# Performance work log

Measured on AMD Instinct MI355X. Metric: run time of the kernel, lower is better.

## Reference

```python
import jax, jax.numpy as jnp
import numpy as np

# TT factorization: vocab = 8*8*8*8*16 = 65536, dim = 4^5 = 1024, rank 16
SHAPE = [(8, 4), (8, 4), (8, 4), (8, 4), (16, 4)]
RANKS = [1, 16, 16, 16, 16, 1]
VOCAB = 65536
DIM = 1024
BATCH, SEQ = 8, 2048


def setup_inputs() -> dict:
    key = jax.random.key(0)
    ks = jax.random.split(key, len(SHAPE) + 1)
    inp = {}
    for k, (n, m) in enumerate(SHAPE):
        core = jax.random.normal(ks[k], (RANKS[k], n * m, RANKS[k + 1]), dtype=jnp.float32) * 0.01
        inp[f"core{k}"] = core
    inp["indices"] = jax.random.randint(ks[-1], (BATCH, SEQ), 0, VOCAB)
    return inp


def _tt_full(cores):
    # Faithful port of tt_to_matrix: chain matmul of cores, then a flat reshape
    # to (VOCAB, DIM).  (The original code reshapes merged_shape -> (rows, cols)
    # directly, without the inverse interleave permute; we replicate that.)
    result = cores[0]  # (1, n0*m0, r1)
    for core in cores[1:]:
        r_prev = result.shape[-1]
        result = (result.reshape(-1, r_prev) @ core.reshape(r_prev, -1))
        result = result.reshape(1, -1, core.shape[-1])
    return result.reshape(VOCAB, DIM)


def reference(core0, core1, core2, core3, core4, indices):
    full = _tt_full([core0, core1, core2, core3, core4])  # (VOCAB, DIM)
    return jnp.take(full, indices, axis=0)              # (BATCH, SEQ, DIM)
```

## Files before the change

kernel.cpp:

```cpp
#include <hip/hip_runtime.h>
#include <hip/hip_fp16.h>


typedef float f32x4 __attribute__((ext_vector_type(4)));

#define RSTRIDE 20
#define GSTRIDE 328

__global__ __launch_bounds__(256) void tt_embed_kernel(
    const float* __restrict__ c0,
    const float* __restrict__ c1,
    const float* __restrict__ c2,
    const float* __restrict__ c3,
    const float* __restrict__ c4,
    const int*   __restrict__ idx,
    float*       __restrict__ out,
    int n_tokens)
{
    const int t   = threadIdx.x;
    const int tl  = t >> 5;
    const int l32 = t & 31;
    const int h   = (t >> 4) & 1;
    const int r   = t & 15;
    const int token = blockIdx.x * 8 + tl;
    const int v = (token < n_tokens) ? idx[token] : 0;

    __shared__ float w4s[8 * GSTRIDE];

    __half2 c4h[16][2];
    #pragma unroll
    for (int r4 = 0; r4 < 16; ++r4) {
        const float4 cv = *(const float4*)(c4 + (r4 << 6) + (r << 2));
        c4h[r4][0] = __floats2half2_rn(cv.x, cv.y);
        c4h[r4][1] = __floats2half2_rn(cv.z, cv.w);
    }

    float w2r = 0.f;
    {
        const int i0 = (v >> 11) & 31;
        const int i1 = (v >> 6) & 31;
        #pragma unroll
        for (int r1 = 0; r1 < 16; ++r1)
            w2r = fmaf(c0[i0 * 16 + r1], c1[(r1 * 32 + i1) * 16 + r], w2r);
    }

    float w3r = 0.f;
    {
        const int i2 = (v >> 1) & 31;
        #pragma unroll
        for (int r2 = 0; r2 < 16; ++r2)
            w3r = fmaf(__shfl(w2r, r2, 16), c2[(r2 * 32 + i2) * 16 + r], w3r);
    }

    {
        const int vlow16 = (v & 1) << 4;
        float4 a0 = {0,0,0,0}, a1 = {0,0,0,0};
        #pragma unroll
        for (int r3 = 0; r3 < 16; ++r3) {
            const float wv = __shfl(w3r, r3, 16);
            const float* base = c3 + ((r3 * 32 + vlow16) << 4);
            const float4 b0 = *(const float4*)(base + (l32 << 2));
            const float4 b1 = *(const float4*)(base + 128 + (l32 << 2));
            a0.x = fmaf(wv, b0.x, a0.x); a0.y = fmaf(wv, b0.y, a0.y);
            a0.z = fmaf(wv, b0.z, a0.z); a0.w = fmaf(wv, b0.w, a0.w);
            a1.x = fmaf(wv, b1.x, a1.x); a1.y = fmaf(wv, b1.y, a1.y);
            a1.z = fmaf(wv, b1.z, a1.z); a1.w = fmaf(wv, b1.w, a1.w);
        }
        float* sb = &w4s[tl * GSTRIDE + ((l32 & 3) << 2)];
        *(float4*)(sb + ( (l32 >> 2)     ) * RSTRIDE) = a0;
        *(float4*)(sb + ( 8 + (l32 >> 2) ) * RSTRIDE) = a1;
    }

    {
        float* outp = out + (size_t)token * 1024 + (r << 2);
        const float* slab = &w4s[tl * GSTRIDE];

        #pragma unroll
        for (int j = 0; j < 8; ++j) {
            const int k = 2 * j + h;
            const float4* wrp = (const float4*)(slab + k * RSTRIDE);
            float wr[16];
            *(float4*)&wr[0]  = wrp[0];
            *(float4*)&wr[4]  = wrp[1];
            *(float4*)&wr[8]  = wrp[2];
            *(float4*)&wr[12] = wrp[3];

            float4 acc = {0,0,0,0};
            #pragma unroll
            for (int r4 = 0; r4 < 16; ++r4) {
                const float cx = __half2float(c4h[r4][0].x);
                const float cy = __half2float(c4h[r4][0].y);
                const float cz = __half2float(c4h[r4][1].x);
                const float cw = __half2float(c4h[r4][1].y);
                acc.x = fmaf(wr[r4], cx, acc.x);
                acc.y = fmaf(wr[r4], cy, acc.y);
                acc.z = fmaf(wr[r4], cz, acc.z);
                acc.w = fmaf(wr[r4], cw, acc.w);
            }

            if (token < n_tokens)
                __builtin_nontemporal_store(*(const f32x4*)&acc,
                                            (f32x4*)(outp + (k << 6)));
        }
    }
}

extern "C" void kernel_launch(void* const* d_in, const int* in_sizes, int n_in,
                              void* d_out, int out_size, void* d_ws, size_t ws_size,
                              hipStream_t stream) {
    const float* c0  = (const float*)d_in[0];
    const float* c1  = (const float*)d_in[1];
    const float* c2  = (const float*)d_in[2];
    const float* c3  = (const float*)d_in[3];
    const float* c4  = (const float*)d_in[4];
    const int*   idx = (const int*)d_in[5];
    float* out = (float*)d_out;

    const int n_tokens = in_sizes[5];
    const int grid = (n_tokens + 7) / 8;
    tt_embed_kernel<<<grid, 256, 0, stream>>>(c0, c1, c2, c3, c4, idx, out, n_tokens);
}
```

Before: 26.56 us.

## Remap final stage so each wavefront lane writes one scalar column per token

The final contraction with core4 is remapped so each 64-lane wavefront handles two tokens. Each lane owns one of the 64 output columns and keeps those 16 core4 values in fp32 registers, replacing the half-precision packing. The stores become scalar nontemporal writes, one dword per lane per row, instead of float4 per lane. Launch bounds now request 8 blocks per multiprocessor to cut register use and raise occupancy. This drops the fp16 conversions and some register pressure, but issues four times as many store instructions.

```diff
diff --git a/kernel.cpp b/kernel.cpp
--- a/kernel.cpp
+++ b/kernel.cpp
@@ -1,13 +1,11 @@
 #include <hip/hip_runtime.h>
-#include <hip/hip_fp16.h>
+#include <hip/hip_bf16.h>
 
-
-typedef float f32x4 __attribute__((ext_vector_type(4)));
 
 #define RSTRIDE 20
 #define GSTRIDE 328
 
-__global__ __launch_bounds__(256) void tt_embed_kernel(
+__global__ __launch_bounds__(256, 8) void tt_embed_kernel(
     const float* __restrict__ c0,
     const float* __restrict__ c1,
     const float* __restrict__ c2,
@@ -20,20 +18,18 @@
     const int t   = threadIdx.x;
     const int tl  = t >> 5;
     const int l32 = t & 31;
-    const int h   = (t >> 4) & 1;
     const int r   = t & 15;
+    const int l   = t & 63;
+    const int wid = t >> 6;
     const int token = blockIdx.x * 8 + tl;
     const int v = (token < n_tokens) ? idx[token] : 0;
 
     __shared__ float w4s[8 * GSTRIDE];
 
-    __half2 c4h[16][2];
+    float c4v[16];
     #pragma unroll
-    for (int r4 = 0; r4 < 16; ++r4) {
-        const float4 cv = *(const float4*)(c4 + (r4 << 6) + (r << 2));
-        c4h[r4][0] = __floats2half2_rn(cv.x, cv.y);
-        c4h[r4][1] = __floats2half2_rn(cv.z, cv.w);
-    }
+    for (int r4 = 0; r4 < 16; ++r4)
+        c4v[r4] = c4[(r4 << 6) + l];
 
     float w2r = 0.f;
     {
@@ -67,40 +63,42 @@
             a1.z = fmaf(wv, b1.z, a1.z); a1.w = fmaf(wv, b1.w, a1.w);
         }
         float* sb = &w4s[tl * GSTRIDE + ((l32 & 3) << 2)];
-        *(float4*)(sb + ( (l32 >> 2)     ) * RSTRIDE) = a0;
-        *(float4*)(sb + ( 8 + (l32 >> 2) ) * RSTRIDE) = a1;
+        *(float4*)(sb + ((l32 >> 2)    ) * RSTRIDE) = a0;
+        *(float4*)(sb + (8 + (l32 >> 2)) * RSTRIDE) = a1;
     }
 
-    {
-        float* outp = out + (size_t)token * 1024 + (r << 2);
-        const float* slab = &w4s[tl * GSTRIDE];
+    #pragma unroll
+    for (int s = 0; s < 2; ++s) {
+        const int slot = 2 * wid + s;
+        const int tok  = blockIdx.x * 8 + slot;
+        const float* slab = &w4s[slot * GSTRIDE];
+        float* outp = out + (size_t)tok * 1024 + l;
 
         #pragma unroll
-        for (int j = 0; j < 8; ++j) {
-            const int k = 2 * j + h;
-            const float4* wrp = (const float4*)(slab + k * RSTRIDE);
-            float wr[16];
-            *(float4*)&wr[0]  = wrp[0];
-            *(float4*)&wr[4]  = wrp[1];
-            *(float4*)&wr[8]  = wrp[2];
-            *(float4*)&wr[12] = wrp[3];
+        for (int k = 0; k < 16; ++k) {
+            const float4* wp = (const float4*)(slab + k * RSTRIDE);
+            const float4 wa = wp[0], wb = wp[1], wc = wp[2], wd = wp[3];
 
-            float4 acc = {0,0,0,0};
-            #pragma unroll
-            for (int r4 = 0; r4 < 16; ++r4) {
-                const float cx = __half2float(c4h[r4][0].x);
-                const float cy = __half2float(c4h[r4][0].y);
-                const float cz = __half2float(c4h[r4][1].x);
-                const float cw = __half2float(c4h[r4][1].y);
-                acc.x = fmaf(wr[r4], cx, acc.x);
-                acc.y = fmaf(wr[r4], cy, acc.y);
-                acc.z = fmaf(wr[r4], cz, acc.z);
-                acc.w = fmaf(wr[r4], cw, acc.w);
-            }
+            float acc = 0.f;
+            acc = fmaf(wa.x, c4v[ 0], acc);
+            acc = fmaf(wa.y, c4v[ 1], acc);
+            acc = fmaf(wa.z, c4v[ 2], acc);
+            acc = fmaf(wa.w, c4v[ 3], acc);
+            acc = fmaf(wb.x, c4v[ 4], acc);
+            acc = fmaf(wb.y, c4v[ 5], acc);
+            acc = fmaf(wb.z, c4v[ 6], acc);
+            acc = fmaf(wb.w, c4v[ 7], acc);
+            acc = fmaf(wc.x, c4v[ 8], acc);
+            acc = fmaf(wc.y, c4v[ 9], acc);
+            acc = fmaf(wc.z, c4v[10], acc);
+            acc = fmaf(wc.w, c4v[11], acc);
+            acc = fmaf(wd.x, c4v[12], acc);
+            acc = fmaf(wd.y, c4v[13], acc);
+            acc = fmaf(wd.z, c4v[14], acc);
+            acc = fmaf(wd.w, c4v[15], acc);
 
-            if (token < n_tokens)
-                __builtin_nontemporal_store(*(const f32x4*)&acc,
-                                            (f32x4*)(outp + (k << 6)));
+            if (tok < n_tokens)
+                __builtin_nontemporal_store(acc, outp + (k << 6));
         }
     }
 }
```

After: 26.59 us. About the same (+0.1%).
